# Kernel tuning notes

Hardware: AMD Instinct MI355X
Metric: run time of the kernel (lower is better)

The kernel has to match this reference:

```python
import jax, jax.numpy as jnp
import numpy as np

BATCH = 16384
N_MODES = 4096  # grid length == retained Fourier modes


def setup_inputs() -> dict:
    key = jax.random.key(0)
    k1, k2, k3 = jax.random.split(key, 3)
    inputs = jax.random.normal(k1, (BATCH, N_MODES), dtype=jnp.float32)
    # he_normal-style init for fourier weights, normal for linear weights
    fourier_weights = jax.random.normal(k2, (N_MODES,), dtype=jnp.float32) * np.sqrt(2.0 / N_MODES).astype(np.float32)
    linear_weights = jax.random.normal(k3, (N_MODES,), dtype=jnp.float32)
    return {"inputs": inputs, "fourier_weights": fourier_weights, "linear_weights": linear_weights}


def reference(inputs, fourier_weights, linear_weights):
    n_modes = fourier_weights.shape[0]
    # FFT along last axis (tf.signal.fft semantics), truncate to n_modes
    xf = jnp.fft.fft(inputs.astype(jnp.complex64), axis=-1)[:, :n_modes]
    # complex elementwise multiply by real weights cast to complex
    xf = xf * fourier_weights.astype(jnp.complex64)
    # inverse FFT over the truncated spectrum, take real part
    x = jnp.real(jnp.fft.ifft(xf, axis=-1)).astype(jnp.float32)
    # spectral branch scaled by linear weights + linear skip branch
    x = x * linear_weights
    z = inputs * linear_weights
    return jax.nn.relu(x + z)
```

## Files before the change

kernel.cpp:

```cpp
#include <hip/hip_runtime.h>
#include <math.h>

#define FFT_N   4096
#define THREADS 256
#define PADN    4352

__device__ __forceinline__ int pad4(int i) { return i + 4 * (i >> 6); }

#define REV(r) ((((r) & 3) << 2) | ((r) >> 2))

__global__ void setup_g_kernel(const float* __restrict__ fw, float* __restrict__ gperm) {
    int p = blockIdx.x * blockDim.x + threadIdx.x;
    if (p >= FFT_N) return;
    int r = p & 15;
    int local = (p & ~15) | REV(r);
    unsigned k = ((local & 15u) << 8) | ((unsigned)local & 0xF0u) | ((unsigned)local >> 8);
    float wk  = fw[k];
    float wnk = fw[(FFT_N - k) & (FFT_N - 1)];
    gperm[p] = (0.5f * (wk + wnk) + 1.0f) * (1.0f / (float)FFT_N);
}

__device__ __forceinline__ void cmul(float& xr, float& xi, float c, float s) {
    float tv = xr; xr = tv * c - xi * s; xi = tv * s + xi * c;
}

__device__ __forceinline__ void bfly4_f(float& ar, float& ai, float& br, float& bi,
                                        float& cr, float& ci, float& dr, float& di) {
    float t0r = ar + cr, t0i = ai + ci;
    float t1r = ar - cr, t1i = ai - ci;
    float t2r = br + dr, t2i = bi + di;
    float t3r = br - dr, t3i = bi - di;
    ar = t0r + t2r; ai = t0i + t2i;
    br = t1r + t3i; bi = t1i - t3r;
    cr = t0r - t2r; ci = t0i - t2i;
    dr = t1r - t3i; di = t1i + t3r;
}
__device__ __forceinline__ void bfly4_i(float& ar, float& ai, float& br, float& bi,
                                        float& cr, float& ci, float& dr, float& di) {
    float t0r = ar + cr, t0i = ai + ci;
    float t1r = ar - cr, t1i = ai - ci;
    float t2r = br + dr, t2i = bi + di;
    float t3r = br - dr, t3i = bi - di;
    ar = t0r + t2r; ai = t0i + t2i;
    br = t1r - t3i; bi = t1i + t3r;
    cr = t0r - t2r; ci = t0i - t2i;
    dr = t1r + t3i; di = t1i - t3r;
}

__device__ __forceinline__ void dft16_f(float xr[16], float xi[16]) {
    const float C1 = 0.9238795325112867f;
    const float S1 = 0.3826834323650898f;
    const float H  = 0.7071067811865476f;
    #pragma unroll
    for (int m = 0; m < 4; ++m)
        bfly4_f(xr[m],xi[m], xr[m+4],xi[m+4], xr[m+8],xi[m+8], xr[m+12],xi[m+12]);
    cmul(xr[5],  xi[5],   C1, -S1);
    cmul(xr[9],  xi[9],    H,  -H);
    cmul(xr[13], xi[13],  S1, -C1);
    cmul(xr[6],  xi[6],    H,  -H);
    cmul(xr[10], xi[10], 0.f, -1.f);
    cmul(xr[14], xi[14],  -H,  -H);
    cmul(xr[7],  xi[7],   S1, -C1);
    cmul(xr[11], xi[11],  -H,  -H);
    cmul(xr[15], xi[15], -C1,  S1);
    #pragma unroll
    for (int g = 0; g < 4; ++g)
        bfly4_f(xr[4*g],xi[4*g], xr[4*g+1],xi[4*g+1], xr[4*g+2],xi[4*g+2], xr[4*g+3],xi[4*g+3]);
}

__device__ __forceinline__ void idft16(float xr[16], float xi[16]) {
    const float C1 = 0.9238795325112867f;
    const float S1 = 0.3826834323650898f;
    const float H  = 0.7071067811865476f;
    #pragma unroll
    for (int g = 0; g < 4; ++g)
        bfly4_i(xr[4*g],xi[4*g], xr[4*g+1],xi[4*g+1], xr[4*g+2],xi[4*g+2], xr[4*g+3],xi[4*g+3]);
    cmul(xr[5],  xi[5],   C1,  S1);
    cmul(xr[9],  xi[9],    H,   H);
    cmul(xr[13], xi[13],  S1,  C1);
    cmul(xr[6],  xi[6],    H,   H);
    cmul(xr[10], xi[10], 0.f, 1.f);
    cmul(xr[14], xi[14],  -H,   H);
    cmul(xr[7],  xi[7],   S1,  C1);
    cmul(xr[11], xi[11],  -H,   H);
    cmul(xr[15], xi[15], -C1, -S1);
    #pragma unroll
    for (int m = 0; m < 4; ++m)
        bfly4_i(xr[m],xi[m], xr[m+4],xi[m+4], xr[m+8],xi[m+8], xr[m+12],xi[m+12]);
}

__device__ __forceinline__ void twiddle_rev(float xr[16], float xi[16], float ang) {
    float s1, c1; __sincosf(ang, &s1, &c1);
    float c2 = c1*c1 - s1*s1, s2 = 2.f*c1*s1;
    float c3 = c2*c1 - s2*s1, s3 = c2*s1 + s2*c1;
    float c4 = c2*c2 - s2*s2, s4 = 2.f*c2*s2;
    cmul(xr[4],  xi[4],  c1, s1);
    cmul(xr[8],  xi[8],  c2, s2);
    cmul(xr[12], xi[12], c3, s3);
    float bc = c4, bs = s4;
    #pragma unroll
    for (int q = 1; q < 4; ++q) {
        cmul(xr[q], xi[q], bc, bs);
        { float ec = bc*c1 - bs*s1, es = bc*s1 + bs*c1; cmul(xr[4+q],  xi[4+q],  ec, es); }
        { float ec = bc*c2 - bs*s2, es = bc*s2 + bs*c2; cmul(xr[8+q],  xi[8+q],  ec, es); }
        { float ec = bc*c3 - bs*s3, es = bc*s3 + bs*c3; cmul(xr[12+q], xi[12+q], ec, es); }
        if (q < 3) { float nb = bc*c4 - bs*s4; bs = bc*s4 + bs*c4; bc = nb; }
    }
}

__global__ __launch_bounds__(THREADS, 4) void fourier_fft_kernel(
    const float* __restrict__ in, const float* __restrict__ gperm,
    const float* __restrict__ lw, float* __restrict__ out)
{
    __shared__ float re[PADN];
    __shared__ float im[PADN];
    const int t = threadIdx.x;
    const long long pair = blockIdx.x;
    const float* r0 = in + pair * (2LL * FFT_N);
    const float* r1 = r0 + FFT_N;

    const float CFA = -6.28318530717958647692f / 4096.0f;
    const float CFB = -6.28318530717958647692f / 256.0f;

    const int baseA = t + 4 * (t >> 6);
    const int baseB = 272 * (t >> 4) + (t & 15);
    const int baseC = 16 * t + 4 * (t >> 2);
    const int jb = t & 15;

    float xr[16], xi[16];

    #pragma unroll
    for (int n = 0; n < 16; ++n) {
        xr[n] = r0[t + 256*n];
        xi[n] = r1[t + 256*n];
    }

    dft16_f(xr, xi);
    twiddle_rev(xr, xi, CFA * (float)t);
    #pragma unroll
    for (int k = 0; k < 16; ++k) {
        int s = baseA + 272*k;
        re[s] = xr[REV(k)]; im[s] = xi[REV(k)];
    }
    __syncthreads();

    #pragma unroll
    for (int n = 0; n < 16; ++n) {
        int s = baseB + 16*n + 4*(n>>2);
        xr[n] = re[s]; xi[n] = im[s];
    }
    dft16_f(xr, xi);
    twiddle_rev(xr, xi, CFB * (float)jb);
    #pragma unroll
    for (int k = 0; k < 16; ++k) {
        int s = baseB + 16*k + 4*(k>>2);
        re[s] = xr[REV(k)]; im[s] = xi[REV(k)];
    }
    __syncthreads();

    #pragma unroll
    for (int q = 0; q < 4; ++q) {
        float4 vr = *(const float4*)&re[baseC + 4*q];
        float4 vi = *(const float4*)&im[baseC + 4*q];
        xr[4*q+0] = vr.x; xr[4*q+1] = vr.y; xr[4*q+2] = vr.z; xr[4*q+3] = vr.w;
        xi[4*q+0] = vi.x; xi[4*q+1] = vi.y; xi[4*q+2] = vi.z; xi[4*q+3] = vi.w;
    }
    dft16_f(xr, xi);
    {
        const float4* gp = (const float4*)(gperm + 16*t);
        #pragma unroll
        for (int q = 0; q < 4; ++q) {
            float4 g = gp[q];
            xr[4*q+0] *= g.x; xi[4*q+0] *= g.x;
            xr[4*q+1] *= g.y; xi[4*q+1] *= g.y;
            xr[4*q+2] *= g.z; xi[4*q+2] *= g.z;
            xr[4*q+3] *= g.w; xi[4*q+3] *= g.w;
        }
    }
    idft16(xr, xi);
    #pragma unroll
    for (int q = 0; q < 4; ++q) {
        *(float4*)&re[baseC + 4*q] = make_float4(xr[4*q+0], xr[4*q+1], xr[4*q+2], xr[4*q+3]);
        *(float4*)&im[baseC + 4*q] = make_float4(xi[4*q+0], xi[4*q+1], xi[4*q+2], xi[4*q+3]);
    }
    __syncthreads();

    #pragma unroll
    for (int k = 0; k < 16; ++k) {
        int s = baseB + 16*k + 4*(k>>2);
        xr[REV(k)] = re[s]; xi[REV(k)] = im[s];
    }
    twiddle_rev(xr, xi, -CFB * (float)jb);
    idft16(xr, xi);
    #pragma unroll
    for (int n = 0; n < 16; ++n) {
        int s = baseB + 16*n + 4*(n>>2);
        re[s] = xr[n]; im[s] = xi[n];
    }
    __syncthreads();

    #pragma unroll
    for (int k = 0; k < 16; ++k) {
        int s = baseA + 272*k;
        xr[REV(k)] = re[s]; xi[REV(k)] = im[s];
    }
    twiddle_rev(xr, xi, -CFA * (float)t);
    idft16(xr, xi);

    float* o0 = out + pair * (2LL * FFT_N);
    #pragma unroll
    for (int n = 0; n < 16; ++n) {
        int i = t + 256*n;
        float l = lw[i];
        o0[i]         = fmaxf(xr[n]*l, 0.0f);
        o0[FFT_N + i] = fmaxf(xi[n]*l, 0.0f);
    }
}

extern "C" void kernel_launch(void* const* d_in, const int* in_sizes, int n_in,
                              void* d_out, int out_size, void* d_ws, size_t ws_size,
                              hipStream_t stream) {
    const float* inputs = (const float*)d_in[0];
    const float* fw     = (const float*)d_in[1];
    const float* lw     = (const float*)d_in[2];
    float* out   = (float*)d_out;
    float* gperm = (float*)d_ws;

    hipLaunchKernelGGL(setup_g_kernel, dim3(FFT_N / THREADS), dim3(THREADS), 0, stream,
                       fw, gperm);

    const int pairs = in_sizes[0] / (2 * FFT_N);
    hipLaunchKernelGGL(fourier_fft_kernel, dim3(pairs), dim3(THREADS), 0, stream,
                       inputs, gperm, lw, out);
}
```

Before: 116.3 us.

## Remap shared-memory FFT transposes so middle stages use float4 LDS accesses

Changes the shared-memory index mapping across the five-stage FFT/IFFT pipeline. The second forward stage and the second-to-last inverse stage now read and write 16-byte vectors instead of scalar strided accesses, and the third stage moves to scalar reads. The arrays are also explicitly 16-byte aligned. The intent is to cut LDS instruction count and bank conflicts in the transposes, at the cost of a different conflict pattern on the scalar-access stages.

Result: slower. 119.5 us (+2.8%).

```diff
diff --git a/kernel.cpp b/kernel.cpp
--- a/kernel.cpp
+++ b/kernel.cpp
@@ -5,7 +5,6 @@
 #define THREADS 256
 #define PADN    4352
 
-__device__ __forceinline__ int pad4(int i) { return i + 4 * (i >> 6); }
 
 #define REV(r) ((((r) & 3) << 2) | ((r) >> 2))
 
@@ -112,8 +111,8 @@
     const float* __restrict__ in, const float* __restrict__ gperm,
     const float* __restrict__ lw, float* __restrict__ out)
 {
-    __shared__ float re[PADN];
-    __shared__ float im[PADN];
+    __shared__ __align__(16) float re[PADN];
+    __shared__ __align__(16) float im[PADN];
     const int t = threadIdx.x;
     const long long pair = blockIdx.x;
     const float* r0 = in + pair * (2LL * FFT_N);
@@ -122,10 +121,10 @@
     const float CFA = -6.28318530717958647692f / 4096.0f;
     const float CFB = -6.28318530717958647692f / 256.0f;
 
-    const int baseA = t + 4 * (t >> 6);
-    const int baseB = 272 * (t >> 4) + (t & 15);
-    const int baseC = 16 * t + 4 * (t >> 2);
-    const int jb = t & 15;
+    const int jt = t & 15, ht = t >> 4;
+    const int baseL = 16*jt + 4*(jt>>2) + ht;
+    const int baseB = 272*ht + 16*jt + 4*(jt>>2);
+    const int baseC = 272*ht + jt;
 
     float xr[16], xi[16];
 
@@ -139,31 +138,31 @@
     twiddle_rev(xr, xi, CFA * (float)t);
     #pragma unroll
     for (int k = 0; k < 16; ++k) {
-        int s = baseA + 272*k;
-        re[s] = xr[REV(k)]; im[s] = xi[REV(k)];
-    }
-    __syncthreads();
-
-    #pragma unroll
-    for (int n = 0; n < 16; ++n) {
-        int s = baseB + 16*n + 4*(n>>2);
-        xr[n] = re[s]; xi[n] = im[s];
-    }
-    dft16_f(xr, xi);
-    twiddle_rev(xr, xi, CFB * (float)jb);
-    #pragma unroll
-    for (int k = 0; k < 16; ++k) {
-        int s = baseB + 16*k + 4*(k>>2);
-        re[s] = xr[REV(k)]; im[s] = xi[REV(k)];
-    }
-    __syncthreads();
-
-    #pragma unroll
-    for (int q = 0; q < 4; ++q) {
-        float4 vr = *(const float4*)&re[baseC + 4*q];
-        float4 vi = *(const float4*)&im[baseC + 4*q];
+        re[baseL + 272*k] = xr[REV(k)];
+        im[baseL + 272*k] = xi[REV(k)];
+    }
+    __syncthreads();
+
+    #pragma unroll
+    for (int q = 0; q < 4; ++q) {
+        float4 vr = *(const float4*)&re[baseB + 4*q];
+        float4 vi = *(const float4*)&im[baseB + 4*q];
         xr[4*q+0] = vr.x; xr[4*q+1] = vr.y; xr[4*q+2] = vr.z; xr[4*q+3] = vr.w;
         xi[4*q+0] = vi.x; xi[4*q+1] = vi.y; xi[4*q+2] = vi.z; xi[4*q+3] = vi.w;
+    }
+    dft16_f(xr, xi);
+    twiddle_rev(xr, xi, CFB * (float)jt);
+    #pragma unroll
+    for (int q = 0; q < 4; ++q) {
+        *(float4*)&re[baseB + 4*q] = make_float4(xr[q], xr[4+q], xr[8+q], xr[12+q]);
+        *(float4*)&im[baseB + 4*q] = make_float4(xi[q], xi[4+q], xi[8+q], xi[12+q]);
+    }
+    __syncthreads();
+
+    #pragma unroll
+    for (int n = 0; n < 16; ++n) {
+        int s = baseC + 16*n + 4*(n>>2);
+        xr[n] = re[s]; xi[n] = im[s];
     }
     dft16_f(xr, xi);
     {
@@ -179,30 +178,32 @@
     }
     idft16(xr, xi);
     #pragma unroll
-    for (int q = 0; q < 4; ++q) {
-        *(float4*)&re[baseC + 4*q] = make_float4(xr[4*q+0], xr[4*q+1], xr[4*q+2], xr[4*q+3]);
-        *(float4*)&im[baseC + 4*q] = make_float4(xi[4*q+0], xi[4*q+1], xi[4*q+2], xi[4*q+3]);
+    for (int n = 0; n < 16; ++n) {
+        int s = baseC + 16*n + 4*(n>>2);
+        re[s] = xr[n]; im[s] = xi[n];
+    }
+    __syncthreads();
+
+    #pragma unroll
+    for (int q = 0; q < 4; ++q) {
+        float4 vr = *(const float4*)&re[baseB + 4*q];
+        float4 vi = *(const float4*)&im[baseB + 4*q];
+        xr[q] = vr.x; xr[4+q] = vr.y; xr[8+q] = vr.z; xr[12+q] = vr.w;
+        xi[q] = vi.x; xi[4+q] = vi.y; xi[8+q] = vi.z; xi[12+q] = vi.w;
+    }
+    twiddle_rev(xr, xi, -CFB * (float)jt);
+    idft16(xr, xi);
+    #pragma unroll
+    for (int q = 0; q < 4; ++q) {
+        *(float4*)&re[baseB + 4*q] = make_float4(xr[4*q+0], xr[4*q+1], xr[4*q+2], xr[4*q+3]);
+        *(float4*)&im[baseB + 4*q] = make_float4(xi[4*q+0], xi[4*q+1], xi[4*q+2], xi[4*q+3]);
     }
     __syncthreads();
 
     #pragma unroll
     for (int k = 0; k < 16; ++k) {
-        int s = baseB + 16*k + 4*(k>>2);
-        xr[REV(k)] = re[s]; xi[REV(k)] = im[s];
-    }
-    twiddle_rev(xr, xi, -CFB * (float)jb);
-    idft16(xr, xi);
-    #pragma unroll
-    for (int n = 0; n < 16; ++n) {
-        int s = baseB + 16*n + 4*(n>>2);
-        re[s] = xr[n]; im[s] = xi[n];
-    }
-    __syncthreads();
-
-    #pragma unroll
-    for (int k = 0; k < 16; ++k) {
-        int s = baseA + 272*k;
-        xr[REV(k)] = re[s]; xi[REV(k)] = im[s];
+        xr[REV(k)] = re[baseL + 272*k];
+        xi[REV(k)] = im[baseL + 272*k];
     }
     twiddle_rev(xr, xi, -CFA * (float)t);
     idft16(xr, xi);
```

## Use persistent grid with register prefetch of next row pair

Applied to the files above, without the earlier changes.

Replaces the one-block-per-pair launch with a persistent grid of 768 blocks that loop over pairs. While the first FFT stage finishes, each block prefetches the next pair's input into registers so global load latency overlaps compute. Occupancy hint drops from 4 to 3 blocks per CU because of the extra 32 prefetch registers. The pair count is now hardcoded (NPAIRS) instead of derived from the input size, which fixes the kernel to the test shape.

Result: slower. 311.6 us (+167.9%).

```diff
diff --git a/kernel.cpp b/kernel.cpp
--- a/kernel.cpp
+++ b/kernel.cpp
@@ -4,8 +4,9 @@
 #define FFT_N   4096
 #define THREADS 256
 #define PADN    4352
-
-__device__ __forceinline__ int pad4(int i) { return i + 4 * (i >> 6); }
+#define GRID    768
+#define NPAIRS  8192
+
 
 #define REV(r) ((((r) & 3) << 2) | ((r) >> 2))
 
@@ -108,16 +109,13 @@
     }
 }
 
-__global__ __launch_bounds__(THREADS, 4) void fourier_fft_kernel(
+__global__ __launch_bounds__(THREADS, 3) void fourier_fft_kernel(
     const float* __restrict__ in, const float* __restrict__ gperm,
     const float* __restrict__ lw, float* __restrict__ out)
 {
-    __shared__ float re[PADN];
-    __shared__ float im[PADN];
+    __shared__ __align__(16) float re[PADN];
+    __shared__ __align__(16) float im[PADN];
     const int t = threadIdx.x;
-    const long long pair = blockIdx.x;
-    const float* r0 = in + pair * (2LL * FFT_N);
-    const float* r1 = r0 + FFT_N;
 
     const float CFA = -6.28318530717958647692f / 4096.0f;
     const float CFB = -6.28318530717958647692f / 256.0f;
@@ -127,93 +125,125 @@
     const int baseC = 16 * t + 4 * (t >> 2);
     const int jb = t & 15;
 
+    const float angA_f =  CFA * (float)t;
+    const float angB_f =  CFB * (float)jb;
+
     float xr[16], xi[16];
-
-    #pragma unroll
-    for (int n = 0; n < 16; ++n) {
-        xr[n] = r0[t + 256*n];
-        xi[n] = r1[t + 256*n];
+    float pr[16], pi[16];
+
+    long long pair = blockIdx.x;
+
+    {
+        const float* r0 = in + pair * (2LL * FFT_N);
+        const float* r1 = r0 + FFT_N;
+        #pragma unroll
+        for (int n = 0; n < 16; ++n) {
+            xr[n] = r0[t + 256*n];
+            xi[n] = r1[t + 256*n];
+        }
     }
 
-    dft16_f(xr, xi);
-    twiddle_rev(xr, xi, CFA * (float)t);
-    #pragma unroll
-    for (int k = 0; k < 16; ++k) {
-        int s = baseA + 272*k;
-        re[s] = xr[REV(k)]; im[s] = xi[REV(k)];
-    }
-    __syncthreads();
-
-    #pragma unroll
-    for (int n = 0; n < 16; ++n) {
-        int s = baseB + 16*n + 4*(n>>2);
-        xr[n] = re[s]; xi[n] = im[s];
-    }
-    dft16_f(xr, xi);
-    twiddle_rev(xr, xi, CFB * (float)jb);
-    #pragma unroll
-    for (int k = 0; k < 16; ++k) {
-        int s = baseB + 16*k + 4*(k>>2);
-        re[s] = xr[REV(k)]; im[s] = xi[REV(k)];
-    }
-    __syncthreads();
-
-    #pragma unroll
-    for (int q = 0; q < 4; ++q) {
-        float4 vr = *(const float4*)&re[baseC + 4*q];
-        float4 vi = *(const float4*)&im[baseC + 4*q];
-        xr[4*q+0] = vr.x; xr[4*q+1] = vr.y; xr[4*q+2] = vr.z; xr[4*q+3] = vr.w;
-        xi[4*q+0] = vi.x; xi[4*q+1] = vi.y; xi[4*q+2] = vi.z; xi[4*q+3] = vi.w;
-    }
-    dft16_f(xr, xi);
-    {
-        const float4* gp = (const float4*)(gperm + 16*t);
+    while (true) {
+        const long long nxt = pair + GRID;
+        const bool has_next = (nxt < NPAIRS);
+
+        dft16_f(xr, xi);
+        twiddle_rev(xr, xi, angA_f);
+        #pragma unroll
+        for (int k = 0; k < 16; ++k) {
+            re[baseA + 272*k] = xr[REV(k)];
+            im[baseA + 272*k] = xi[REV(k)];
+        }
+        if (has_next) {
+            const float* r0 = in + nxt * (2LL * FFT_N);
+            const float* r1 = r0 + FFT_N;
+            #pragma unroll
+            for (int n = 0; n < 16; ++n) {
+                pr[n] = r0[t + 256*n];
+                pi[n] = r1[t + 256*n];
+            }
+        }
+        __syncthreads();
+
+        #pragma unroll
+        for (int n = 0; n < 16; ++n) {
+            int s = baseB + 16*n + 4*(n>>2);
+            xr[n] = re[s]; xi[n] = im[s];
+        }
+        dft16_f(xr, xi);
+        twiddle_rev(xr, xi, angB_f);
+        #pragma unroll
+        for (int k = 0; k < 16; ++k) {
+            int s = baseB + 16*k + 4*(k>>2);
+            re[s] = xr[REV(k)]; im[s] = xi[REV(k)];
+        }
+        __syncthreads();
+
         #pragma unroll
         for (int q = 0; q < 4; ++q) {
-            float4 g = gp[q];
-            xr[4*q+0] *= g.x; xi[4*q+0] *= g.x;
-            xr[4*q+1] *= g.y; xi[4*q+1] *= g.y;
-            xr[4*q+2] *= g.z; xi[4*q+2] *= g.z;
-            xr[4*q+3] *= g.w; xi[4*q+3] *= g.w;
-        }
-    }
-    idft16(xr, xi);
-    #pragma unroll
-    for (int q = 0; q < 4; ++q) {
-        *(float4*)&re[baseC + 4*q] = make_float4(xr[4*q+0], xr[4*q+1], xr[4*q+2], xr[4*q+3]);
-        *(float4*)&im[baseC + 4*q] = make_float4(xi[4*q+0], xi[4*q+1], xi[4*q+2], xi[4*q+3]);
-    }
-    __syncthreads();
-
-    #pragma unroll
-    for (int k = 0; k < 16; ++k) {
-        int s = baseB + 16*k + 4*(k>>2);
-        xr[REV(k)] = re[s]; xi[REV(k)] = im[s];
-    }
-    twiddle_rev(xr, xi, -CFB * (float)jb);
-    idft16(xr, xi);
-    #pragma unroll
-    for (int n = 0; n < 16; ++n) {
-        int s = baseB + 16*n + 4*(n>>2);
-        re[s] = xr[n]; im[s] = xi[n];
-    }
-    __syncthreads();
-
-    #pragma unroll
-    for (int k = 0; k < 16; ++k) {
-        int s = baseA + 272*k;
-        xr[REV(k)] = re[s]; xi[REV(k)] = im[s];
-    }
-    twiddle_rev(xr, xi, -CFA * (float)t);
-    idft16(xr, xi);
-
-    float* o0 = out + pair * (2LL * FFT_N);
-    #pragma unroll
-    for (int n = 0; n < 16; ++n) {
-        int i = t + 256*n;
-        float l = lw[i];
-        o0[i]         = fmaxf(xr[n]*l, 0.0f);
-        o0[FFT_N + i] = fmaxf(xi[n]*l, 0.0f);
+            float4 vr = *(const float4*)&re[baseC + 4*q];
+            float4 vi = *(const float4*)&im[baseC + 4*q];
+            xr[4*q+0] = vr.x; xr[4*q+1] = vr.y; xr[4*q+2] = vr.z; xr[4*q+3] = vr.w;
+            xi[4*q+0] = vi.x; xi[4*q+1] = vi.y; xi[4*q+2] = vi.z; xi[4*q+3] = vi.w;
+        }
+        dft16_f(xr, xi);
+        {
+            const float4* gp = (const float4*)(gperm + 16*t);
+            #pragma unroll
+            for (int q = 0; q < 4; ++q) {
+                float4 g = gp[q];
+                xr[4*q+0] *= g.x; xi[4*q+0] *= g.x;
+                xr[4*q+1] *= g.y; xi[4*q+1] *= g.y;
+                xr[4*q+2] *= g.z; xi[4*q+2] *= g.z;
+                xr[4*q+3] *= g.w; xi[4*q+3] *= g.w;
+            }
+        }
+        idft16(xr, xi);
+        #pragma unroll
+        for (int q = 0; q < 4; ++q) {
+            *(float4*)&re[baseC + 4*q] = make_float4(xr[4*q+0], xr[4*q+1], xr[4*q+2], xr[4*q+3]);
+            *(float4*)&im[baseC + 4*q] = make_float4(xi[4*q+0], xi[4*q+1], xi[4*q+2], xi[4*q+3]);
+        }
+        __syncthreads();
+
+        #pragma unroll
+        for (int k = 0; k < 16; ++k) {
+            int s = baseB + 16*k + 4*(k>>2);
+            xr[REV(k)] = re[s]; xi[REV(k)] = im[s];
+        }
+        twiddle_rev(xr, xi, -angB_f);
+        idft16(xr, xi);
+        #pragma unroll
+        for (int n = 0; n < 16; ++n) {
+            int s = baseB + 16*n + 4*(n>>2);
+            re[s] = xr[n]; im[s] = xi[n];
+        }
+        __syncthreads();
+
+        #pragma unroll
+        for (int k = 0; k < 16; ++k) {
+            xr[REV(k)] = re[baseA + 272*k];
+            xi[REV(k)] = im[baseA + 272*k];
+        }
+        twiddle_rev(xr, xi, -angA_f);
+        idft16(xr, xi);
+
+        {
+            float* o0 = out + pair * (2LL * FFT_N);
+            #pragma unroll
+            for (int n = 0; n < 16; ++n) {
+                int i = t + 256*n;
+                float l = lw[i];
+                o0[i]         = fmaxf(xr[n]*l, 0.0f);
+                o0[FFT_N + i] = fmaxf(xi[n]*l, 0.0f);
+            }
+        }
+
+        if (!has_next) break;
+        #pragma unroll
+        for (int n = 0; n < 16; ++n) { xr[n] = pr[n]; xi[n] = pi[n]; }
+        pair = nxt;
+        __syncthreads();
     }
 }
 
@@ -229,7 +259,6 @@
     hipLaunchKernelGGL(setup_g_kernel, dim3(FFT_N / THREADS), dim3(THREADS), 0, stream,
                        fw, gperm);
 
-    const int pairs = in_sizes[0] / (2 * FFT_N);
-    hipLaunchKernelGGL(fourier_fft_kernel, dim3(pairs), dim3(THREADS), 0, stream,
+    hipLaunchKernelGGL(fourier_fft_kernel, dim3(GRID), dim3(THREADS), 0, stream,
                        inputs, gperm, lw, out);
 }
```
